# Kernel optimization log

Hardware: AMD Instinct MI355X
Metric: run time of the kernel (lower is better)

## Reference

```python
import jax, jax.numpy as jnp
import numpy as np

EMB = 128  # embsize
WORD = 128  # word_size
ITERS = 2


def _agg(embeds, neibors):
    # embeds: [B, N, D], neibors: [B, N, K] indices into node axis N (per batch)
    # mean-pool gathered neighbor embeddings -> [B, N, D]
    gathered = jax.vmap(lambda e, idx: e[idx])(embeds, neibors)  # [B, N, K, D]
    return gathered.mean(axis=2)


def setup_inputs() -> dict:
    key = jax.random.key(0)
    ks = jax.random.split(key, 9)
    B, N, K = 64, 512, 16
    word_embs = jax.random.normal(ks[0], (B, N, WORD), dtype=jnp.float32)
    lib_embs = jax.random.normal(ks[1], (B, N, WORD), dtype=jnp.float32)
    neibors = jax.random.randint(ks[2], (B, N, K), 0, N)
    neibors_lib = jax.random.randint(ks[3], (B, N, K), 0, N)
    mask = jax.random.uniform(ks[4], (B, N), dtype=jnp.float32)
    # xavier-uniform style params
    def xav(k, shape):
        bound = float(np.sqrt(6.0 / (shape[0] + shape[1])))
        return jax.random.uniform(k, shape, dtype=jnp.float32, minval=-bound, maxval=bound)
    weight = xav(ks[5], (WORD, EMB))
    weight2 = xav(ks[6], (EMB, EMB))
    enc_w1 = xav(ks[7], (WORD, EMB))
    enc_w2 = xav(ks[8], (EMB, EMB))
    return {"word_embs": word_embs, "neibors": neibors, "lib_embs": lib_embs,
            "neibors_lib": neibors_lib, "mask": mask, "weight": weight,
            "weight2": weight2, "enc_w1": enc_w1, "enc_w2": enc_w2}


def reference(word_embs, neibors, lib_embs, neibors_lib, mask, weight, weight2, enc_w1, enc_w2):
    B, N, _ = word_embs.shape
    # lib aggregation is loop-invariant (lib_embs fixed); same math as in-loop recompute
    agg_lib = jnp.einsum('bnw,we->bne', _agg(lib_embs, neibors_lib), weight)  # [B, N, EMB]
    word_proj = jnp.einsum('bnw,we->bne', word_embs, enc_w1)  # loop-invariant
    last_embed = jnp.zeros((B, N, EMB), dtype=jnp.float32)
    for _ in range(ITERS):
        agg_func = _agg(last_embed, neibors)  # [B, N, EMB]
        last_embed = jnp.tanh(word_proj + jnp.einsum('bne,ef->bnf', agg_func, enc_w2) + agg_lib)
    # masked sum over nodes, then final linear
    pooled = (last_embed * mask[:, :, None]).sum(axis=1)  # [B, EMB]
    return pooled @ weight2
```

## Files before the change

kernel.cpp:

```cpp
#include <hip/hip_runtime.h>
#include <hip/hip_bf16.h>

#define B_   64
#define N_   512
#define K_   16
#define D_   128
#define NPB  16
#define G1   ((B_*N_)/NPB)

typedef float f32x4  __attribute__((ext_vector_type(4)));
typedef short bf16x8 __attribute__((ext_vector_type(8)));

static __device__ __forceinline__ short f2bf(float x) {
    union { float f; unsigned u; } v; v.f = x;
    unsigned r = v.u + 0x7fffu + ((v.u >> 16) & 1u);
    return (short)(r >> 16);
}
static __device__ __forceinline__ float bf2f(short h) {
    return __uint_as_float(((unsigned)(unsigned short)h) << 16);
}
static __device__ __forceinline__ float fast_tanh(float x) {
    float e = __expf(2.f * x);
    return 1.f - 2.f * __builtin_amdgcn_rcpf(e + 1.f);
}
static __device__ __forceinline__ void pk_add(float2& acc, float x, float y) {
    float2 v; v.x = x; v.y = y;
    asm("v_pk_add_f32 %0, %1, %0" : "+v"(acc) : "v"(v));
}

__global__ __launch_bounds__(256) void pack(const float* __restrict__ enc1,
                                            const float* __restrict__ wgt,
                                            const float* __restrict__ enc2,
                                            short* __restrict__ Bp1,
                                            short* __restrict__ Bp2,
                                            float* __restrict__ out) {
    const int blk = blockIdx.x, t = threadIdx.x;
    if (blk >= 24) { out[(blk - 24) * 256 + t] = 0.f; return; }
    int tid = blk * 256 + t;
    short o8[8];
    if (tid < 4096) {
        int l = tid & 63, nt = (tid >> 6) & 7, ks = tid >> 9;
        int k0 = ks * 32 + (l >> 4) * 8;
        int col = nt * 16 + (l & 15);
#pragma unroll
        for (int j = 0; j < 8; ++j) {
            int r = k0 + j;
            float v = (r < 128) ? enc1[r * 128 + col] : wgt[(r - 128) * 128 + col];
            o8[j] = f2bf(v);
        }
        *(int4*)&Bp1[(size_t)tid * 8] = *(int4*)o8;
    } else {
        int t2 = tid - 4096;
        int l = t2 & 63, nt = (t2 >> 6) & 7, ks = t2 >> 9;
        int k0 = ks * 32 + (l >> 4) * 8;
        int col = nt * 16 + (l & 15);
#pragma unroll
        for (int j = 0; j < 8; ++j) o8[j] = f2bf(enc2[(k0 + j) * 128 + col]);
        *(int4*)&Bp2[(size_t)t2 * 8] = *(int4*)o8;
    }
}

static __device__ __forceinline__ int swz_blk() {
    const int hw = blockIdx.x;
    return ((hw & 7) << 8) + (hw >> 3);
}

#define LDA1 264
#define LDA2 136

__global__ __launch_bounds__(256) void gemm1(const float* __restrict__ word,
                                             const int* __restrict__ nbrL,
                                             const float* __restrict__ lib,
                                             const short* __restrict__ Bp1,
                                             short* __restrict__ baseh,
                                             float* __restrict__ t1f) {
    __shared__ short sA[NPB * LDA1];
    __shared__ int sIdx[NPB * 16];
    const int tid = threadIdx.x;
    const int blk = swz_blk();
    const int b = blk >> 5;
    const int node0 = blk * NPB;

    if (tid < 64) *(int4*)&sIdx[tid * 4] = *(const int4*)&nbrL[(size_t)node0 * 16 + tid * 4];
    __syncthreads();

    const int w = tid >> 6, l = tid & 63;
    const int rh = l >> 5, c4 = l & 31;
    const float* libB = lib + (size_t)b * N_ * D_;

#pragma unroll
    for (int p = 0; p < 2; ++p) {
        const int row = 4 * w + 2 * p + rh;
        const int gid = node0 + row;
        float4 wv = *(const float4*)&word[(size_t)gid * D_ + c4 * 4];
        short4 ws; ws.x = f2bf(wv.x); ws.y = f2bf(wv.y); ws.z = f2bf(wv.z); ws.w = f2bf(wv.w);
        *(short4*)&sA[row * LDA1 + c4 * 4] = ws;
        int idxr[16];
#pragma unroll
        for (int q = 0; q < 4; ++q) *(int4*)&idxr[q * 4] = *(const int4*)&sIdx[row * 16 + q * 4];
        float2 a01 = {0.f, 0.f}, a23 = {0.f, 0.f};
#pragma unroll
        for (int k = 0; k < 16; ++k) {
            float4 lv = *(const float4*)&libB[(size_t)idxr[k] * D_ + c4 * 4];
            pk_add(a01, lv.x, lv.y);
            pk_add(a23, lv.z, lv.w);
        }
        short4 as; as.x = f2bf(a01.x * 0.0625f); as.y = f2bf(a01.y * 0.0625f);
        as.z = f2bf(a23.x * 0.0625f); as.w = f2bf(a23.y * 0.0625f);
        *(short4*)&sA[row * LDA1 + 128 + c4 * 4] = as;
    }
    __syncthreads();

    f32x4 acc[2];
    acc[0] = (f32x4)0.f; acc[1] = (f32x4)0.f;
    const int arow = l & 15;
#pragma unroll
    for (int ks = 0; ks < 8; ++ks) {
        bf16x8 a = *(const bf16x8*)&sA[arow * LDA1 + ks * 32 + (l >> 4) * 8];
#pragma unroll
        for (int j = 0; j < 2; ++j) {
            const int nt = 2 * w + j;
            bf16x8 bb = *(const bf16x8*)&Bp1[((size_t)(ks * 8 + nt) * 64 + l) * 8];
            acc[j] = __builtin_amdgcn_mfma_f32_16x16x32_bf16(a, bb, acc[j], 0, 0, 0);
        }
    }

    const int r0 = (l >> 4) * 4;
    const int cl = l & 15;
#pragma unroll
    for (int j = 0; j < 2; ++j) {
        const int col = (2 * w + j) * 16 + cl;
#pragma unroll
        for (int r = 0; r < 4; ++r) {
            size_t o = (size_t)(node0 + r0 + r) * D_ + col;
            float v = acc[j][r];
            baseh[o] = f2bf(v);
            t1f[o]   = fast_tanh(v);
        }
    }
}

__global__ __launch_bounds__(256) void gemm2(const float* __restrict__ t1f,
                                             const int* __restrict__ nbr,
                                             const short* __restrict__ Bp2,
                                             const short* __restrict__ baseh,
                                             const float* __restrict__ mask,
                                             const float* __restrict__ w2,
                                             float* __restrict__ out) {
    __shared__ short sA[NPB * LDA2];
    __shared__ int sIdx[NPB * 16];
    __shared__ float pred[128];
    __shared__ float smask[NPB];
    const int tid = threadIdx.x;
    const int blk = swz_blk();
    const int b = blk >> 5;
    const int node0 = blk * NPB;

    if (tid < 64) *(int4*)&sIdx[tid * 4] = *(const int4*)&nbr[(size_t)node0 * 16 + tid * 4];
    if (tid >= 64 && tid < 64 + NPB) smask[tid - 64] = mask[node0 + tid - 64];
    __syncthreads();

    const int w = tid >> 6, l = tid & 63;
    const int rh = l >> 5, c4 = l & 31;
    const float* t1B = t1f + (size_t)b * N_ * D_;

#pragma unroll
    for (int p = 0; p < 2; ++p) {
        const int row = 4 * w + 2 * p + rh;
        int idxr[16];
#pragma unroll
        for (int q = 0; q < 4; ++q) *(int4*)&idxr[q * 4] = *(const int4*)&sIdx[row * 16 + q * 4];
        float2 a01 = {0.f, 0.f}, a23 = {0.f, 0.f};
#pragma unroll
        for (int k = 0; k < 16; ++k) {
            float4 lv = *(const float4*)&t1B[(size_t)idxr[k] * D_ + c4 * 4];
            pk_add(a01, lv.x, lv.y);
            pk_add(a23, lv.z, lv.w);
        }
        short4 as; as.x = f2bf(a01.x * 0.0625f); as.y = f2bf(a01.y * 0.0625f);
        as.z = f2bf(a23.x * 0.0625f); as.w = f2bf(a23.y * 0.0625f);
        *(short4*)&sA[row * LDA2 + c4 * 4] = as;
    }
    __syncthreads();

    f32x4 acc[2];
    acc[0] = (f32x4)0.f; acc[1] = (f32x4)0.f;
    const int arow = l & 15;
#pragma unroll
    for (int ks = 0; ks < 4; ++ks) {
        bf16x8 a = *(const bf16x8*)&sA[arow * LDA2 + ks * 32 + (l >> 4) * 8];
#pragma unroll
        for (int j = 0; j < 2; ++j) {
            const int nt = 2 * w + j;
            bf16x8 bb = *(const bf16x8*)&Bp2[((size_t)(ks * 8 + nt) * 64 + l) * 8];
            acc[j] = __builtin_amdgcn_mfma_f32_16x16x32_bf16(a, bb, acc[j], 0, 0, 0);
        }
    }

    const int r0 = (l >> 4) * 4;
    const int cl = l & 15;
#pragma unroll
    for (int j = 0; j < 2; ++j) {
        const int col = (2 * w + j) * 16 + cl;
        float s = 0.f;
#pragma unroll
        for (int r = 0; r < 4; ++r) {
            size_t o = (size_t)(node0 + r0 + r) * D_ + col;
            float v = fast_tanh(bf2f(baseh[o]) + acc[j][r]);
            s += v * smask[r0 + r];
        }
        s += __shfl_xor(s, 16);
        s += __shfl_xor(s, 32);
        if (l < 16) pred[col] = s;
    }
    __syncthreads();
    if (tid < 128) {
        float a2 = 0.f;
#pragma unroll 4
        for (int f = 0; f < 128; ++f) a2 += pred[f] * w2[f * 128 + tid];
        atomicAdd(&out[b * 128 + tid], a2);
    }
}

extern "C" void kernel_launch(void* const* d_in, const int* in_sizes, int n_in,
                              void* d_out, int out_size, void* d_ws, size_t ws_size,
                              hipStream_t stream) {
    const float* word_embs   = (const float*)d_in[0];
    const int*   neibors     = (const int*)d_in[1];
    const float* lib_embs    = (const float*)d_in[2];
    const int*   neibors_lib = (const int*)d_in[3];
    const float* mask        = (const float*)d_in[4];
    const float* weight      = (const float*)d_in[5];
    const float* weight2     = (const float*)d_in[6];
    const float* enc_w1      = (const float*)d_in[7];
    const float* enc_w2      = (const float*)d_in[8];
    float* out = (float*)d_out;

    char* ws = (char*)d_ws;
    short* baseh = (short*)(ws);
    float* t1f   = (float*)(ws + (1u << 23));
    short* Bp1   = (short*)(ws + (3u << 23));
    short* Bp2   = (short*)(ws + (3u << 23) + 65536);

    pack<<<56, 256, 0, stream>>>(enc_w1, weight, enc_w2, Bp1, Bp2, out);
    gemm1<<<G1, 256, 0, stream>>>(word_embs, neibors_lib, lib_embs, Bp1, baseh, t1f);
    gemm2<<<G1, 256, 0, stream>>>(t1f, neibors, Bp2, baseh, mask, weight2, out);
}
```

Before: 53.47 us.

## Stage batch embeddings in LDS and fold neighbor mean into per-neighbor MFMA

Each block now covers 128 nodes with 512 threads. It first copies the whole batch's lib or t1 embeddings (as bf16) into a swizzled 128KB LDS buffer. Neighbor aggregation is no longer a scalar gather-and-mean followed by a GEMM: each neighbor's row is fed straight into MFMA against a weight pre-scaled by 1/16. This turns the scattered global gathers into LDS reads. The cost is 16x more MFMA work for the aggregation term, the full batch being reloaded four times (once per block), and only one block fitting per CU because of the LDS footprint. The intermediate t1 is also stored as bf16 instead of fp32, halving that traffic.

```diff
diff --git a/kernel.cpp b/kernel.cpp
--- a/kernel.cpp
+++ b/kernel.cpp
@@ -1,12 +1,12 @@
 #include <hip/hip_runtime.h>
 #include <hip/hip_bf16.h>
 
-#define B_   64
-#define N_   512
-#define K_   16
-#define D_   128
-#define NPB  16
-#define G1   ((B_*N_)/NPB)
+#define B_    64
+#define N_    512
+#define K_    16
+#define D_    128
+#define NPBLK 128
+#define GG    ((B_*N_)/NPBLK)
 
 typedef float f32x4  __attribute__((ext_vector_type(4)));
 typedef short bf16x8 __attribute__((ext_vector_type(8)));
@@ -23,201 +23,215 @@
     float e = __expf(2.f * x);
     return 1.f - 2.f * __builtin_amdgcn_rcpf(e + 1.f);
 }
-static __device__ __forceinline__ void pk_add(float2& acc, float x, float y) {
-    float2 v; v.x = x; v.y = y;
-    asm("v_pk_add_f32 %0, %1, %0" : "+v"(acc) : "v"(v));
-}
 
 __global__ __launch_bounds__(256) void pack(const float* __restrict__ enc1,
                                             const float* __restrict__ wgt,
                                             const float* __restrict__ enc2,
-                                            short* __restrict__ Bp1,
+                                            short* __restrict__ Bp1e,
+                                            short* __restrict__ Bpw,
                                             short* __restrict__ Bp2,
                                             float* __restrict__ out) {
     const int blk = blockIdx.x, t = threadIdx.x;
     if (blk >= 24) { out[(blk - 24) * 256 + t] = 0.f; return; }
-    int tid = blk * 256 + t;
+    const int ptid = blk * 256 + t;
+    const int m3 = ptid >> 11;
+    const int r = ptid & 2047;
+    const int ks = r >> 9, nt = (r >> 6) & 7, l = r & 63;
+    const int k0 = ks * 32 + (l >> 4) * 8;
+    const int col = nt * 16 + (l & 15);
+    const float* src = (m3 == 0) ? enc1 : (m3 == 1) ? wgt : enc2;
+    const float scale = (m3 == 0) ? 1.0f : 0.0625f;
+    short* dst = (m3 == 0) ? Bp1e : (m3 == 1) ? Bpw : Bp2;
     short o8[8];
-    if (tid < 4096) {
-        int l = tid & 63, nt = (tid >> 6) & 7, ks = tid >> 9;
-        int k0 = ks * 32 + (l >> 4) * 8;
-        int col = nt * 16 + (l & 15);
-#pragma unroll
-        for (int j = 0; j < 8; ++j) {
-            int r = k0 + j;
-            float v = (r < 128) ? enc1[r * 128 + col] : wgt[(r - 128) * 128 + col];
-            o8[j] = f2bf(v);
-        }
-        *(int4*)&Bp1[(size_t)tid * 8] = *(int4*)o8;
-    } else {
-        int t2 = tid - 4096;
-        int l = t2 & 63, nt = (t2 >> 6) & 7, ks = t2 >> 9;
-        int k0 = ks * 32 + (l >> 4) * 8;
-        int col = nt * 16 + (l & 15);
-#pragma unroll
-        for (int j = 0; j < 8; ++j) o8[j] = f2bf(enc2[(k0 + j) * 128 + col]);
-        *(int4*)&Bp2[(size_t)t2 * 8] = *(int4*)o8;
-    }
+#pragma unroll
+    for (int j = 0; j < 8; ++j) o8[j] = f2bf(src[(k0 + j) * 128 + col] * scale);
+    *(int4*)&dst[(size_t)r * 8] = *(int4*)o8;
 }
 
 static __device__ __forceinline__ int swz_blk() {
     const int hw = blockIdx.x;
-    return ((hw & 7) << 8) + (hw >> 3);
-}
-
-#define LDA1 264
-#define LDA2 136
-
-__global__ __launch_bounds__(256) void gemm1(const float* __restrict__ word,
+    return ((hw & 7) << 5) + (hw >> 3);
+}
+
+static __device__ __forceinline__ int lds_addr(int row, int colb) {
+    return (row * 256 + colb) ^ ((row & 7) << 4);
+}
+
+__global__ __launch_bounds__(512, 2) void g1(const float* __restrict__ word,
                                              const int* __restrict__ nbrL,
                                              const float* __restrict__ lib,
-                                             const short* __restrict__ Bp1,
+                                             const short* __restrict__ Bp1e,
+                                             const short* __restrict__ Bpw,
                                              short* __restrict__ baseh,
-                                             float* __restrict__ t1f) {
-    __shared__ short sA[NPB * LDA1];
-    __shared__ int sIdx[NPB * 16];
+                                             short* __restrict__ t1g) {
+    extern __shared__ char smem[];
+    short* sM  = (short*)smem;
+    int*  sIdx = (int*)(smem + 131072);
     const int tid = threadIdx.x;
-    const int blk = swz_blk();
-    const int b = blk >> 5;
-    const int node0 = blk * NPB;
-
-    if (tid < 64) *(int4*)&sIdx[tid * 4] = *(const int4*)&nbrL[(size_t)node0 * 16 + tid * 4];
+    const int logical = swz_blk();
+    const int b = logical >> 2;
+    const int node0 = (logical & 3) * NPBLK;
+    const int gnode0 = b * N_ + node0;
+
+    const float* libB = lib + (size_t)b * N_ * D_;
+#pragma unroll 4
+    for (int it = 0; it < 32; ++it) {
+        const int i = it * 2048 + tid * 4;
+        float4 v = *(const float4*)&libB[i];
+        short4 s; s.x = f2bf(v.x); s.y = f2bf(v.y); s.z = f2bf(v.z); s.w = f2bf(v.w);
+        *(short4*)(smem + lds_addr(i >> 7, (i & 127) * 2)) = s;
+    }
+    *(int4*)&sIdx[tid * 4] = *(const int4*)&nbrL[(size_t)gnode0 * 16 + tid * 4];
     __syncthreads();
 
     const int w = tid >> 6, l = tid & 63;
-    const int rh = l >> 5, c4 = l & 31;
-    const float* libB = lib + (size_t)b * N_ * D_;
-
-#pragma unroll
-    for (int p = 0; p < 2; ++p) {
-        const int row = 4 * w + 2 * p + rh;
-        const int gid = node0 + row;
-        float4 wv = *(const float4*)&word[(size_t)gid * D_ + c4 * 4];
-        short4 ws; ws.x = f2bf(wv.x); ws.y = f2bf(wv.y); ws.z = f2bf(wv.z); ws.w = f2bf(wv.w);
-        *(short4*)&sA[row * LDA1 + c4 * 4] = ws;
-        int idxr[16];
-#pragma unroll
-        for (int q = 0; q < 4; ++q) *(int4*)&idxr[q * 4] = *(const int4*)&sIdx[row * 16 + q * 4];
-        float2 a01 = {0.f, 0.f}, a23 = {0.f, 0.f};
-#pragma unroll
-        for (int k = 0; k < 16; ++k) {
-            float4 lv = *(const float4*)&libB[(size_t)idxr[k] * D_ + c4 * 4];
-            pk_add(a01, lv.x, lv.y);
-            pk_add(a23, lv.z, lv.w);
-        }
-        short4 as; as.x = f2bf(a01.x * 0.0625f); as.y = f2bf(a01.y * 0.0625f);
-        as.z = f2bf(a23.x * 0.0625f); as.w = f2bf(a23.y * 0.0625f);
-        *(short4*)&sA[row * LDA1 + 128 + c4 * 4] = as;
-    }
-    __syncthreads();
-
-    f32x4 acc[2];
-    acc[0] = (f32x4)0.f; acc[1] = (f32x4)0.f;
-    const int arow = l & 15;
-#pragma unroll
-    for (int ks = 0; ks < 8; ++ks) {
-        bf16x8 a = *(const bf16x8*)&sA[arow * LDA1 + ks * 32 + (l >> 4) * 8];
-#pragma unroll
-        for (int j = 0; j < 2; ++j) {
-            const int nt = 2 * w + j;
-            bf16x8 bb = *(const bf16x8*)&Bp1[((size_t)(ks * 8 + nt) * 64 + l) * 8];
-            acc[j] = __builtin_amdgcn_mfma_f32_16x16x32_bf16(a, bb, acc[j], 0, 0, 0);
-        }
-    }
-
-    const int r0 = (l >> 4) * 4;
+    const int nrow = w * 16 + (l & 15);
+    int nidx[16];
+#pragma unroll
+    for (int nb = 0; nb < 16; ++nb) nidx[nb] = sIdx[nrow * 16 + nb];
+
+    f32x4 acc[8];
+#pragma unroll
+    for (int nt = 0; nt < 8; ++nt) acc[nt] = (f32x4)0.f;
+
+    bf16x8 bf[32];
+#pragma unroll
+    for (int q = 0; q < 32; ++q) bf[q] = *(const bf16x8*)&Bp1e[(size_t)(q * 64 + l) * 8];
+
+    {
+        const float* wr = word + (size_t)(gnode0 + nrow) * D_ + (l >> 4) * 8;
+#pragma unroll
+        for (int ks = 0; ks < 4; ++ks) {
+            float4 a0 = *(const float4*)&wr[ks * 32];
+            float4 a1 = *(const float4*)&wr[ks * 32 + 4];
+            short af[8];
+            af[0]=f2bf(a0.x); af[1]=f2bf(a0.y); af[2]=f2bf(a0.z); af[3]=f2bf(a0.w);
+            af[4]=f2bf(a1.x); af[5]=f2bf(a1.y); af[6]=f2bf(a1.z); af[7]=f2bf(a1.w);
+            bf16x8 av = *(bf16x8*)af;
+#pragma unroll
+            for (int nt = 0; nt < 8; ++nt)
+                acc[nt] = __builtin_amdgcn_mfma_f32_16x16x32_bf16(av, bf[ks * 8 + nt], acc[nt], 0, 0, 0);
+        }
+    }
+
+#pragma unroll
+    for (int q = 0; q < 32; ++q) bf[q] = *(const bf16x8*)&Bpw[(size_t)(q * 64 + l) * 8];
+
+    const int laneoff = (l >> 4) * 16;
+#pragma unroll
+    for (int nb = 0; nb < 16; ++nb) {
+        const int rbase = nidx[nb] * 256 + laneoff;
+        const int swz = (nidx[nb] & 7) << 4;
+#pragma unroll
+        for (int ksq = 0; ksq < 4; ++ksq) {
+            bf16x8 av = *(const bf16x8*)(smem + ((rbase + ksq * 64) ^ swz));
+#pragma unroll
+            for (int nt = 0; nt < 8; ++nt)
+                acc[nt] = __builtin_amdgcn_mfma_f32_16x16x32_bf16(av, bf[ksq * 8 + nt], acc[nt], 0, 0, 0);
+        }
+    }
+
+    const int r0 = w * 16 + (l >> 4) * 4;
     const int cl = l & 15;
 #pragma unroll
-    for (int j = 0; j < 2; ++j) {
-        const int col = (2 * w + j) * 16 + cl;
+    for (int nt = 0; nt < 8; ++nt) {
+        const int col = nt * 16 + cl;
 #pragma unroll
         for (int r = 0; r < 4; ++r) {
-            size_t o = (size_t)(node0 + r0 + r) * D_ + col;
-            float v = acc[j][r];
+            size_t o = (size_t)(gnode0 + r0 + r) * D_ + col;
+            float v = acc[nt][r];
             baseh[o] = f2bf(v);
-            t1f[o]   = fast_tanh(v);
-        }
-    }
-}
-
-__global__ __launch_bounds__(256) void gemm2(const float* __restrict__ t1f,
+            t1g[o]   = f2bf(fast_tanh(v));
+        }
+    }
+}
+
+__global__ __launch_bounds__(512, 2) void g2(const short* __restrict__ t1g,
                                              const int* __restrict__ nbr,
                                              const short* __restrict__ Bp2,
                                              const short* __restrict__ baseh,
                                              const float* __restrict__ mask,
                                              const float* __restrict__ w2,
                                              float* __restrict__ out) {
-    __shared__ short sA[NPB * LDA2];
-    __shared__ int sIdx[NPB * 16];
-    __shared__ float pred[128];
-    __shared__ float smask[NPB];
+    extern __shared__ char smem[];
+    short* sM   = (short*)smem;
+    int*  sIdx  = (int*)(smem + 131072);
+    float* pred = (float*)(smem + 131072 + 8192);
+    float* ptot = (float*)(smem + 131072 + 8192 + 4096);
+    float* smask= (float*)(smem + 131072 + 8192 + 4096 + 512);
     const int tid = threadIdx.x;
-    const int blk = swz_blk();
-    const int b = blk >> 5;
-    const int node0 = blk * NPB;
-
-    if (tid < 64) *(int4*)&sIdx[tid * 4] = *(const int4*)&nbr[(size_t)node0 * 16 + tid * 4];
-    if (tid >= 64 && tid < 64 + NPB) smask[tid - 64] = mask[node0 + tid - 64];
+    const int logical = swz_blk();
+    const int b = logical >> 2;
+    const int node0 = (logical & 3) * NPBLK;
+    const int gnode0 = b * N_ + node0;
+
+    const short* tB = t1g + (size_t)b * N_ * D_;
+#pragma unroll 4
+    for (int it = 0; it < 16; ++it) {
+        const int i = it * 4096 + tid * 8;
+        int4 v = *(const int4*)&tB[i];
+        *(int4*)(smem + lds_addr(i >> 7, (i & 127) * 2)) = v;
+    }
+    *(int4*)&sIdx[tid * 4] = *(const int4*)&nbr[(size_t)gnode0 * 16 + tid * 4];
+    if (tid < 128) smask[tid] = mask[gnode0 + tid];
     __syncthreads();
 
     const int w = tid >> 6, l = tid & 63;
-    const int rh = l >> 5, c4 = l & 31;
-    const float* t1B = t1f + (size_t)b * N_ * D_;
-
-#pragma unroll
-    for (int p = 0; p < 2; ++p) {
-        const int row = 4 * w + 2 * p + rh;
-        int idxr[16];
-#pragma unroll
-        for (int q = 0; q < 4; ++q) *(int4*)&idxr[q * 4] = *(const int4*)&sIdx[row * 16 + q * 4];
-        float2 a01 = {0.f, 0.f}, a23 = {0.f, 0.f};
-#pragma unroll
-        for (int k = 0; k < 16; ++k) {
-            float4 lv = *(const float4*)&t1B[(size_t)idxr[k] * D_ + c4 * 4];
-            pk_add(a01, lv.x, lv.y);
-            pk_add(a23, lv.z, lv.w);
-        }
-        short4 as; as.x = f2bf(a01.x * 0.0625f); as.y = f2bf(a01.y * 0.0625f);
-        as.z = f2bf(a23.x * 0.0625f); as.w = f2bf(a23.y * 0.0625f);
-        *(short4*)&sA[row * LDA2 + c4 * 4] = as;
-    }
-    __syncthreads();
-
-    f32x4 acc[2];
-    acc[0] = (f32x4)0.f; acc[1] = (f32x4)0.f;
-    const int arow = l & 15;
-#pragma unroll
-    for (int ks = 0; ks < 4; ++ks) {
-        bf16x8 a = *(const bf16x8*)&sA[arow * LDA2 + ks * 32 + (l >> 4) * 8];
-#pragma unroll
-        for (int j = 0; j < 2; ++j) {
-            const int nt = 2 * w + j;
-            bf16x8 bb = *(const bf16x8*)&Bp2[((size_t)(ks * 8 + nt) * 64 + l) * 8];
-            acc[j] = __builtin_amdgcn_mfma_f32_16x16x32_bf16(a, bb, acc[j], 0, 0, 0);
-        }
-    }
-
-    const int r0 = (l >> 4) * 4;
+    const int nrow = w * 16 + (l & 15);
+    int nidx[16];
+#pragma unroll
+    for (int nb = 0; nb < 16; ++nb) nidx[nb] = sIdx[nrow * 16 + nb];
+
+    f32x4 acc[8];
+#pragma unroll
+    for (int nt = 0; nt < 8; ++nt) acc[nt] = (f32x4)0.f;
+
+    bf16x8 bf[32];
+#pragma unroll
+    for (int q = 0; q < 32; ++q) bf[q] = *(const bf16x8*)&Bp2[(size_t)(q * 64 + l) * 8];
+
+    const int laneoff = (l >> 4) * 16;
+#pragma unroll
+    for (int nb = 0; nb < 16; ++nb) {
+        const int rbase = nidx[nb] * 256 + laneoff;
+        const int swz = (nidx[nb] & 7) << 4;
+#pragma unroll
+        for (int ksq = 0; ksq < 4; ++ksq) {
+            bf16x8 av = *(const bf16x8*)(smem + ((rbase + ksq * 64) ^ swz));
+#pragma unroll
+            for (int nt = 0; nt < 8; ++nt)
+                acc[nt] = __builtin_amdgcn_mfma_f32_16x16x32_bf16(av, bf[ksq * 8 + nt], acc[nt], 0, 0, 0);
+        }
+    }
+
+    const int r0 = w * 16 + (l >> 4) * 4;
     const int cl = l & 15;
 #pragma unroll
-    for (int j = 0; j < 2; ++j) {
-        const int col = (2 * w + j) * 16 + cl;
+    for (int nt = 0; nt < 8; ++nt) {
+        const int col = nt * 16 + cl;
         float s = 0.f;
 #pragma unroll
         for (int r = 0; r < 4; ++r) {
-            size_t o = (size_t)(node0 + r0 + r) * D_ + col;
-            float v = fast_tanh(bf2f(baseh[o]) + acc[j][r]);
+            size_t o = (size_t)(gnode0 + r0 + r) * D_ + col;
+            float v = fast_tanh(bf2f(baseh[o]) + acc[nt][r]);
             s += v * smask[r0 + r];
         }
         s += __shfl_xor(s, 16);
         s += __shfl_xor(s, 32);
-        if (l < 16) pred[col] = s;
+        if (l < 16) pred[w * 128 + col] = s;
+    }
+    __syncthreads();
+    if (tid < 128) {
+        float tot = 0.f;
+#pragma unroll
+        for (int i = 0; i < 8; ++i) tot += pred[i * 128 + tid];
+        ptot[tid] = tot;
     }
     __syncthreads();
     if (tid < 128) {
         float a2 = 0.f;
 #pragma unroll 4
-        for (int f = 0; f < 128; ++f) a2 += pred[f] * w2[f * 128 + tid];
+        for (int f = 0; f < 128; ++f) a2 += ptot[f] * w2[f * 128 + tid];
         atomicAdd(&out[b * 128 + tid], a2);
     }
 }
@@ -238,11 +252,17 @@
 
     char* ws = (char*)d_ws;
     short* baseh = (short*)(ws);
-    float* t1f   = (float*)(ws + (1u << 23));
-    short* Bp1   = (short*)(ws + (3u << 23));
-    short* Bp2   = (short*)(ws + (3u << 23) + 65536);
-
-    pack<<<56, 256, 0, stream>>>(enc_w1, weight, enc_w2, Bp1, Bp2, out);
-    gemm1<<<G1, 256, 0, stream>>>(word_embs, neibors_lib, lib_embs, Bp1, baseh, t1f);
-    gemm2<<<G1, 256, 0, stream>>>(t1f, neibors, Bp2, baseh, mask, weight2, out);
-}
+    short* t1g   = (short*)(ws + (1u << 23));
+    short* Bp1e  = (short*)(ws + (2u << 23));
+    short* Bpw   = (short*)(ws + (2u << 23) + 32768);
+    short* Bp2   = (short*)(ws + (2u << 23) + 65536);
+
+    static int attr_done = 0;
+    hipFuncSetAttribute((const void*)g1, hipFuncAttributeMaxDynamicSharedMemorySize, 139264);
+    hipFuncSetAttribute((const void*)g2, hipFuncAttributeMaxDynamicSharedMemorySize, 144896);
+    (void)attr_done;
+
+    pack<<<56, 256, 0, stream>>>(enc_w1, weight, enc_w2, Bp1e, Bpw, Bp2, out);
+    g1<<<GG, 512, 139264, stream>>>(word_embs, neibors_lib, lib_embs, Bp1e, Bpw, baseh, t1g);
+    g2<<<GG, 512, 144896, stream>>>(t1g, neibors, Bp2, baseh, mask, weight2, out);
+}
```

New measurement: 57.35 us. 1.07x slower.
